# Performance work log

Measured on AMD Instinct MI355X. Metric: run time of the kernel, lower is better.

Reference implementation:

```python
import jax, jax.numpy as jnp
import numpy as np

D_MODEL = 1024
N_HEADS = 16
D_K = D_MODEL // N_HEADS


def setup_inputs() -> dict:
    key = jax.random.key(0)
    ks = jax.random.split(key, 7)
    s = 1.0 / np.sqrt(D_MODEL)
    return {
        "x": jax.random.normal(ks[0], (2, 2048, D_MODEL), dtype=jnp.float32),
        "w_q": jax.random.uniform(ks[1], (D_MODEL, D_MODEL), jnp.float32, -s, s),
        "w_k": jax.random.uniform(ks[2], (D_MODEL, D_MODEL), jnp.float32, -s, s),
        "w_v": jax.random.uniform(ks[3], (D_MODEL, D_MODEL), jnp.float32, -s, s),
        "w_o": jax.random.uniform(ks[4], (D_MODEL, D_MODEL), jnp.float32, -s, s),
        "b_o": jax.random.uniform(ks[5], (D_MODEL,), jnp.float32, -s, s),
        "ln_gamma": jnp.ones((D_MODEL,), jnp.float32),
        "ln_beta": jnp.zeros((D_MODEL,), jnp.float32),
    }


def reference(x, w_q, w_k, w_v, w_o, b_o, ln_gamma, ln_beta):
    # Pre-LN
    mu = jnp.mean(x, axis=-1, keepdims=True)
    var = jnp.mean(jnp.square(x - mu), axis=-1, keepdims=True)
    x_norm = (x - mu) / jnp.sqrt(var + 1e-5) * ln_gamma + ln_beta

    B, S, _ = x.shape
    # torch Linear: y = x @ W.T ; weights stored [out, in]
    def proj(w):
        return (x_norm @ w.T).reshape(B, S, N_HEADS, D_K).transpose(0, 2, 1, 3)

    Q, K, V = proj(w_q), proj(w_k), proj(w_v)  # [B,H,S,Dk]
    scores = jnp.einsum("bhqd,bhkd->bhqk", Q, K) / np.sqrt(D_K)
    attn = jax.nn.softmax(scores, axis=-1)
    attended = jnp.einsum("bhqk,bhkd->bhqd", attn, V)
    attended = attended.transpose(0, 2, 1, 3).reshape(B, S, D_MODEL)
    out = attended @ w_o.T + b_o
    return x + out
```

## Files before the change

### kernel.cpp

```cpp
#include <hip/hip_runtime.h>

typedef _Float16 f16;
typedef _Float16 f16x8 __attribute__((ext_vector_type(8)));
typedef _Float16 f16x4 __attribute__((ext_vector_type(4)));
typedef _Float16 f16x2 __attribute__((ext_vector_type(2)));
typedef __fp16 fp16x2 __attribute__((ext_vector_type(2)));
typedef float f32x4 __attribute__((ext_vector_type(4)));

#define SEQ   2048
#define DM    1024
#define DKH   64
#define MTOT  4096

__device__ __forceinline__ f32x4 mfma16(f16x8 a, f16x8 b, f32x4 c) {
  return __builtin_amdgcn_mfma_f32_16x16x32_f16(a, b, c, 0, 0, 0);
}

__device__ __forceinline__ f16x2 cvt_pk(float a, float b) {
  fp16x2 r = __builtin_amdgcn_cvt_pkrtz(a, b);
  return __builtin_bit_cast(f16x2, r);
}

__device__ __forceinline__ void gload16(const f16* g, f16* l) {
  __builtin_amdgcn_global_load_lds(
      (const __attribute__((address_space(1))) void*)g,
      (__attribute__((address_space(3))) void*)l, 16, 0, 0);
}

__global__ __launch_bounds__(256) void prep_kernel(const float* __restrict__ x,
                                                   const float* __restrict__ w_q,
                                                   const float* __restrict__ w_k,
                                                   const float* __restrict__ w_v,
                                                   const float* __restrict__ w_o,
                                                   const float* __restrict__ gamma,
                                                   const float* __restrict__ beta,
                                                   f16* __restrict__ wout,
                                                   f16* __restrict__ xn) {
  const int t = threadIdx.x;
  if (blockIdx.x < 4096) {
    const int sel = blockIdx.x >> 10;
    const float* src = sel == 0 ? w_q : sel == 1 ? w_k : sel == 2 ? w_v : w_o;
    const int i = ((blockIdx.x & 1023) * 256 + t) * 4;
    float4 v = *reinterpret_cast<const float4*>(src + i);
    f16x4 o;
    o[0] = (f16)v.x; o[1] = (f16)v.y; o[2] = (f16)v.z; o[3] = (f16)v.w;
    *reinterpret_cast<f16x4*>(wout + (size_t)sel * 1048576 + i) = o;
    return;
  }
  const int row = blockIdx.x - 4096;
  const float* xr = x + (size_t)row * DM;
  float v[4], s = 0.f, s2 = 0.f;
#pragma unroll
  for (int i = 0; i < 4; ++i) {
    v[i] = xr[t + i * 256];
    s += v[i];
    s2 += v[i] * v[i];
  }
#pragma unroll
  for (int o = 32; o > 0; o >>= 1) {
    s  += __shfl_down(s, o);
    s2 += __shfl_down(s2, o);
  }
  __shared__ float ps[4], ps2[4], mu_s, rs_s;
  if ((t & 63) == 0) { ps[t >> 6] = s; ps2[t >> 6] = s2; }
  __syncthreads();
  if (t == 0) {
    float a = ps[0] + ps[1] + ps[2] + ps[3];
    float b = ps2[0] + ps2[1] + ps2[2] + ps2[3];
    float mu = a * (1.f / DM);
    float var = b * (1.f / DM) - mu * mu;
    mu_s = mu;
    rs_s = rsqrtf(var + 1e-5f);
  }
  __syncthreads();
  const float mu = mu_s, rs = rs_s;
#pragma unroll
  for (int i = 0; i < 4; ++i) {
    int d = t + i * 256;
    xn[(size_t)row * DM + d] = (f16)(((v[i] - mu) * rs) * gamma[d] + beta[d]);
  }
}

__global__ __launch_bounds__(256) void gemm_qkv(const f16* __restrict__ A,
                                                const f16* __restrict__ Wqkv,
                                                f16* __restrict__ qb,
                                                f16* __restrict__ kb,
                                                f16* __restrict__ vtb) {
  __shared__ f16 sA[128][64];
  __shared__ f16 sB[64][64];
  const int t = threadIdx.x, l = t & 63, w = t >> 6;
  const int wr = w >> 1, wc = w & 1, lg = l >> 4, lm = l & 15;
  const int m0 = blockIdx.y * 128, n0 = blockIdx.x * 64;
  const int crow = l >> 3;
  const int scol = ((l & 7) ^ crow) << 3;
  const int rsw  = (lm & 7) << 3;

  f32x4 acc[4][2] = {};

  for (int k0 = 0; k0 < DM; k0 += 64) {
    __syncthreads();
#pragma unroll
    for (int cc = 0; cc < 4; ++cc) {
      const int c = w + cc * 4;
      gload16(A + (size_t)(m0 + c * 8 + crow) * DM + k0 + scol, &sA[c * 8][0]);
    }
#pragma unroll
    for (int cc = 0; cc < 2; ++cc) {
      const int c = w + cc * 4;
      gload16(Wqkv + (size_t)(n0 + c * 8 + crow) * DM + k0 + scol, &sB[c * 8][0]);
    }
    __syncthreads();
#pragma unroll
    for (int kk = 0; kk < 2; ++kk) {
      f16x8 af[4], bf[2];
#pragma unroll
      for (int i = 0; i < 4; ++i)
        af[i] = *(const f16x8*)&sA[wr * 64 + i * 16 + lm][(kk * 32 + lg * 8) ^ rsw];
#pragma unroll
      for (int i = 0; i < 2; ++i)
        bf[i] = *(const f16x8*)&sB[wc * 32 + i * 16 + lm][(kk * 32 + lg * 8) ^ rsw];
#pragma unroll
      for (int mi = 0; mi < 4; ++mi)
#pragma unroll
        for (int ni = 0; ni < 2; ++ni)
          acc[mi][ni] = mfma16(af[mi], bf[ni], acc[mi][ni]);
    }
  }

  const int sel = blockIdx.x >> 4;
  if (sel < 2) {
    f16* outp = sel == 0 ? qb : kb;
    const int nloc = n0 - sel * 1024;
#pragma unroll
    for (int mi = 0; mi < 4; ++mi) {
      const int rowb = m0 + wr * 64 + mi * 16 + lg * 4;
#pragma unroll
      for (int ni = 0; ni < 2; ++ni) {
        const int col = nloc + wc * 32 + ni * 16 + lm;
#pragma unroll
        for (int r = 0; r < 4; ++r)
          outp[(size_t)(rowb + r) * DM + col] = (f16)acc[mi][ni][r];
      }
    }
  } else {
#pragma unroll
    for (int mi = 0; mi < 4; ++mi) {
      const int rowb = m0 + wr * 64 + mi * 16 + lg * 4;
      const int b = rowb >> 11, s = rowb & 2047;
#pragma unroll
      for (int ni = 0; ni < 2; ++ni) {
        const int col = (n0 - 2048) + wc * 32 + ni * 16 + lm;
        f16x4 o;
        o[0] = (f16)acc[mi][ni][0]; o[1] = (f16)acc[mi][ni][1];
        o[2] = (f16)acc[mi][ni][2]; o[3] = (f16)acc[mi][ni][3];
        *reinterpret_cast<f16x4*>(&vtb[(size_t)(b * 1024 + col) * SEQ + s]) = o;
      }
    }
  }
}

__global__ __launch_bounds__(256) void gemm_out(const f16* __restrict__ A,
                                                const f16* __restrict__ W,
                                                float* __restrict__ out,
                                                const float* __restrict__ bias,
                                                const float* __restrict__ resid) {
  __shared__ f16 sA[64][64];
  __shared__ f16 sB[128][64];
  const int t = threadIdx.x, l = t & 63, w = t >> 6;
  const int wr = w >> 1, wc = w & 1, lg = l >> 4, lm = l & 15;
  const int m0 = blockIdx.y * 64, n0 = blockIdx.x * 128;
  const int crow = l >> 3;
  const int scol = ((l & 7) ^ crow) << 3;
  const int rsw  = (lm & 7) << 3;

  f32x4 acc[2][4] = {};

  for (int k0 = 0; k0 < DM; k0 += 64) {
    __syncthreads();
#pragma unroll
    for (int cc = 0; cc < 2; ++cc) {
      const int c = w + cc * 4;
      gload16(A + (size_t)(m0 + c * 8 + crow) * DM + k0 + scol, &sA[c * 8][0]);
    }
#pragma unroll
    for (int cc = 0; cc < 4; ++cc) {
      const int c = w + cc * 4;
      gload16(W + (size_t)(n0 + c * 8 + crow) * DM + k0 + scol, &sB[c * 8][0]);
    }
    __syncthreads();
#pragma unroll
    for (int kk = 0; kk < 2; ++kk) {
      f16x8 af[2], bf[4];
#pragma unroll
      for (int i = 0; i < 2; ++i)
        af[i] = *(const f16x8*)&sA[wr * 32 + i * 16 + lm][(kk * 32 + lg * 8) ^ rsw];
#pragma unroll
      for (int i = 0; i < 4; ++i)
        bf[i] = *(const f16x8*)&sB[wc * 64 + i * 16 + lm][(kk * 32 + lg * 8) ^ rsw];
#pragma unroll
      for (int mi = 0; mi < 2; ++mi)
#pragma unroll
        for (int ni = 0; ni < 4; ++ni)
          acc[mi][ni] = mfma16(af[mi], bf[ni], acc[mi][ni]);
    }
  }

#pragma unroll
  for (int mi = 0; mi < 2; ++mi) {
    const int rowb = m0 + wr * 32 + mi * 16 + lg * 4;
#pragma unroll
    for (int ni = 0; ni < 4; ++ni) {
      const int col = n0 + wc * 64 + ni * 16 + lm;
#pragma unroll
      for (int r = 0; r < 4; ++r) {
        const size_t idx = (size_t)(rowb + r) * DM + col;
        out[idx] = resid[idx] + bias[col] + acc[mi][ni][r];
      }
    }
  }
}

__global__ __launch_bounds__(256) void attn_kernel(const f16* __restrict__ Qb,
                                                   const f16* __restrict__ Kb,
                                                   const f16* __restrict__ Vt,
                                                   f16* __restrict__ Ob) {
  __shared__ f16 sK[2][128][64];
  __shared__ f16 sV[2][64][128];

  int bx = blockIdx.x;
  bx = (bx & 7) * 64 + (bx >> 3);
  const int qt = bx & 15, bh = bx >> 4;
  const int h = bh & 15, b = bh >> 4;
  const int t = threadIdx.x, l = t & 63, w = t >> 6;
  const int lg = l >> 4, lm = l & 15;
  const float K2 = 0.18033688f;

  f16x8 qf[2][2];
#pragma unroll
  for (int qg = 0; qg < 2; ++qg) {
    const f16* qptr =
        Qb + (size_t)(b * SEQ + qt * 128 + w * 32 + qg * 16 + lm) * DM + h * DKH;
    qf[qg][0] = *(const f16x8*)(qptr + lg * 8);
    qf[qg][1] = *(const f16x8*)(qptr + 32 + lg * 8);
#pragma unroll
    for (int j = 0; j < 8; ++j) {
      qf[qg][0][j] = (f16)((float)qf[qg][0][j] * K2);
      qf[qg][1][j] = (f16)((float)qf[qg][1][j] * K2);
    }
  }

  const f16x8 ones = {(f16)1, (f16)1, (f16)1, (f16)1,
                      (f16)1, (f16)1, (f16)1, (f16)1};

  f32x4 oacc[2][4] = {};
  f32x4 oden[2] = {};

  const int crow = l >> 3;
  const int scol = ((l & 7) ^ crow) << 3;
  const int rsw  = (lm & 7) << 3;

  const f16* kptr[4];
  const f16* vptr[4];
#pragma unroll
  for (int cc = 0; cc < 4; ++cc) {
    const int ck = w + cc * 4;
    const int krow = ck * 8 + crow;
    const int half = krow >> 6, r6 = krow & 63;
    const int nfp = r6 >> 4, lgp = (r6 >> 2) & 3, rp = r6 & 3;
    const int key = half * 64 + (nfp >> 1) * 32 + lgp * 8 + (nfp & 1) * 4 + rp;
    kptr[cc] = Kb + (size_t)(b * SEQ + key) * DM + h * DKH + scol;
    const int drow = ck * 4 + (l >> 4);
    const int vcol = ((l & 15) ^ ((ck & 1) * 4 + (l >> 4))) << 3;
    vptr[cc] = Vt + (size_t)(bh * DKH + drow) * SEQ + vcol;
  }

  auto stage = [&](int buf) {
#pragma unroll
    for (int cc = 0; cc < 4; ++cc) {
      const int ck = w + cc * 4;
      gload16(kptr[cc], &sK[buf][ck * 8][0]);
      gload16(vptr[cc], &sV[buf][ck * 4][0]);
      kptr[cc] += 128 * DM;
      vptr[cc] += 128;
    }
  };

  stage(0);
  __syncthreads();
  int cur = 0;

  for (int kt = 0; kt < SEQ / 128; ++kt) {
    if (kt < SEQ / 128 - 1) stage(cur ^ 1);

#pragma unroll
    for (int half = 0; half < 2; ++half) {
      f32x4 sc[2][4] = {};
      __builtin_amdgcn_s_setprio(1);
#pragma unroll
      for (int kk = 0; kk < 2; ++kk)
#pragma unroll
        for (int nf = 0; nf < 4; ++nf) {
          f16x8 kf = *(const f16x8*)
              &sK[cur][half * 64 + nf * 16 + lm][(kk * 32 + lg * 8) ^ rsw];
          sc[0][nf] = mfma16(kf, qf[0][kk], sc[0][nf]);
          sc[1][nf] = mfma16(kf, qf[1][kk], sc[1][nf]);
        }
      __builtin_amdgcn_s_setprio(0);

      union PU { f16x8 v; f16x2 hh[4]; };
      PU pu[2][2];
#pragma unroll
      for (int qg = 0; qg < 2; ++qg)
#pragma unroll
        for (int nf = 0; nf < 4; ++nf) {
          float e0 = __builtin_amdgcn_exp2f(sc[qg][nf][0]);
          float e1 = __builtin_amdgcn_exp2f(sc[qg][nf][1]);
          float e2 = __builtin_amdgcn_exp2f(sc[qg][nf][2]);
          float e3 = __builtin_amdgcn_exp2f(sc[qg][nf][3]);
          pu[qg][nf >> 1].hh[(nf & 1) * 2 + 0] = cvt_pk(e0, e1);
          pu[qg][nf >> 1].hh[(nf & 1) * 2 + 1] = cvt_pk(e2, e3);
        }

      __builtin_amdgcn_s_setprio(1);
#pragma unroll
      for (int ks = 0; ks < 2; ++ks) {
#pragma unroll
        for (int ni = 0; ni < 4; ++ni) {
          f16x8 vf = *(const f16x8*)
              &sV[cur][ni * 16 + lm][(half * 64 + ks * 32 + lg * 8) ^ rsw];
          oacc[0][ni] = mfma16(pu[0][ks].v, vf, oacc[0][ni]);
          oacc[1][ni] = mfma16(pu[1][ks].v, vf, oacc[1][ni]);
        }
        oden[0] = mfma16(pu[0][ks].v, ones, oden[0]);
        oden[1] = mfma16(pu[1][ks].v, ones, oden[1]);
      }
      __builtin_amdgcn_s_setprio(0);
    }

    __syncthreads();
    cur ^= 1;
  }

#pragma unroll
  for (int qg = 0; qg < 2; ++qg) {
    float rd[4];
#pragma unroll
    for (int r = 0; r < 4; ++r) rd[r] = 1.f / oden[qg][r];
#pragma unroll
    for (int ni = 0; ni < 4; ++ni)
#pragma unroll
      for (int r = 0; r < 4; ++r) {
        const int q = qt * 128 + w * 32 + qg * 16 + lg * 4 + r;
        const int d = ni * 16 + lm;
        Ob[(size_t)(b * SEQ + q) * DM + h * DKH + d] = (f16)(oacc[qg][ni][r] * rd[r]);
      }
  }
}

extern "C" void kernel_launch(void* const* d_in, const int* in_sizes, int n_in,
                              void* d_out, int out_size, void* d_ws, size_t ws_size,
                              hipStream_t stream) {
  const float* x   = (const float*)d_in[0];
  const float* w_q = (const float*)d_in[1];
  const float* w_k = (const float*)d_in[2];
  const float* w_v = (const float*)d_in[3];
  const float* w_o = (const float*)d_in[4];
  const float* b_o = (const float*)d_in[5];
  const float* lng = (const float*)d_in[6];
  const float* lnb = (const float*)d_in[7];
  float* out = (float*)d_out;

  char* ws = (char*)d_ws;
  const size_t MB = 1ull << 20;
  f16* xn   = (f16*)(ws + 0 * MB);
  f16* wqkv = (f16*)(ws + 8 * MB);
  f16* woh  = (f16*)(ws + 14 * MB);
  f16* qb   = (f16*)(ws + 16 * MB);
  f16* kb   = (f16*)(ws + 24 * MB);
  f16* vtb  = (f16*)(ws + 32 * MB);
  f16* att  = (f16*)(ws + 40 * MB);

  prep_kernel<<<8192, 256, 0, stream>>>(x, w_q, w_k, w_v, w_o, lng, lnb, wqkv, xn);
  gemm_qkv<<<dim3(48, 32), 256, 0, stream>>>(xn, wqkv, qb, kb, vtb);
  attn_kernel<<<512, 256, 0, stream>>>(qb, kb, vtb, att);
  gemm_out<<<dim3(8, 64), 256, 0, stream>>>(att, woh, out, b_o, x);
}
```

Baseline: 116.4 us.

## Software-pipeline attention halves, split V tile layout, reshape output GEMM tile

The attention inner loop now preloads the K fragments for both 64-key halves and computes the second half's QK^T MFMAs right after the first half's PV MFMAs. This lets the exp work of one half overlap matrix work of the other. The V shared-memory tile is split into two 64x64 halves with a new swizzled staging pattern. The output GEMM switches from 64x128 to 128x64 block tiles with a matching grid. In exchange, register pressure rises from holding 16 K fragments and a second score accumulator, which may lower occupancy.

```diff
diff --git a/kernel.cpp b/kernel.cpp
--- a/kernel.cpp
+++ b/kernel.cpp
@@ -164,53 +164,53 @@
                                                 float* __restrict__ out,
                                                 const float* __restrict__ bias,
                                                 const float* __restrict__ resid) {
-  __shared__ f16 sA[64][64];
-  __shared__ f16 sB[128][64];
+  __shared__ f16 sA[128][64];
+  __shared__ f16 sB[64][64];
   const int t = threadIdx.x, l = t & 63, w = t >> 6;
   const int wr = w >> 1, wc = w & 1, lg = l >> 4, lm = l & 15;
-  const int m0 = blockIdx.y * 64, n0 = blockIdx.x * 128;
+  const int m0 = blockIdx.y * 128, n0 = blockIdx.x * 64;
   const int crow = l >> 3;
   const int scol = ((l & 7) ^ crow) << 3;
   const int rsw  = (lm & 7) << 3;
 
-  f32x4 acc[2][4] = {};
+  f32x4 acc[4][2] = {};
 
   for (int k0 = 0; k0 < DM; k0 += 64) {
     __syncthreads();
 #pragma unroll
+    for (int cc = 0; cc < 4; ++cc) {
+      const int c = w + cc * 4;
+      gload16(A + (size_t)(m0 + c * 8 + crow) * DM + k0 + scol, &sA[c * 8][0]);
+    }
+#pragma unroll
     for (int cc = 0; cc < 2; ++cc) {
       const int c = w + cc * 4;
-      gload16(A + (size_t)(m0 + c * 8 + crow) * DM + k0 + scol, &sA[c * 8][0]);
-    }
-#pragma unroll
-    for (int cc = 0; cc < 4; ++cc) {
-      const int c = w + cc * 4;
       gload16(W + (size_t)(n0 + c * 8 + crow) * DM + k0 + scol, &sB[c * 8][0]);
     }
     __syncthreads();
 #pragma unroll
     for (int kk = 0; kk < 2; ++kk) {
-      f16x8 af[2], bf[4];
+      f16x8 af[4], bf[2];
+#pragma unroll
+      for (int i = 0; i < 4; ++i)
+        af[i] = *(const f16x8*)&sA[wr * 64 + i * 16 + lm][(kk * 32 + lg * 8) ^ rsw];
 #pragma unroll
       for (int i = 0; i < 2; ++i)
-        af[i] = *(const f16x8*)&sA[wr * 32 + i * 16 + lm][(kk * 32 + lg * 8) ^ rsw];
-#pragma unroll
-      for (int i = 0; i < 4; ++i)
-        bf[i] = *(const f16x8*)&sB[wc * 64 + i * 16 + lm][(kk * 32 + lg * 8) ^ rsw];
-#pragma unroll
-      for (int mi = 0; mi < 2; ++mi)
-#pragma unroll
-        for (int ni = 0; ni < 4; ++ni)
+        bf[i] = *(const f16x8*)&sB[wc * 32 + i * 16 + lm][(kk * 32 + lg * 8) ^ rsw];
+#pragma unroll
+      for (int mi = 0; mi < 4; ++mi)
+#pragma unroll
+        for (int ni = 0; ni < 2; ++ni)
           acc[mi][ni] = mfma16(af[mi], bf[ni], acc[mi][ni]);
     }
   }
 
 #pragma unroll
-  for (int mi = 0; mi < 2; ++mi) {
-    const int rowb = m0 + wr * 32 + mi * 16 + lg * 4;
-#pragma unroll
-    for (int ni = 0; ni < 4; ++ni) {
-      const int col = n0 + wc * 64 + ni * 16 + lm;
+  for (int mi = 0; mi < 4; ++mi) {
+    const int rowb = m0 + wr * 64 + mi * 16 + lg * 4;
+#pragma unroll
+    for (int ni = 0; ni < 2; ++ni) {
+      const int col = n0 + wc * 32 + ni * 16 + lm;
 #pragma unroll
       for (int r = 0; r < 4; ++r) {
         const size_t idx = (size_t)(rowb + r) * DM + col;
@@ -225,7 +225,7 @@
                                                    const f16* __restrict__ Vt,
                                                    f16* __restrict__ Ob) {
   __shared__ f16 sK[2][128][64];
-  __shared__ f16 sV[2][64][128];
+  __shared__ f16 sV[2][2][64][64];
 
   int bx = blockIdx.x;
   bx = (bx & 7) * 64 + (bx >> 3);
@@ -269,9 +269,10 @@
     const int nfp = r6 >> 4, lgp = (r6 >> 2) & 3, rp = r6 & 3;
     const int key = half * 64 + (nfp >> 1) * 32 + lgp * 8 + (nfp & 1) * 4 + rp;
     kptr[cc] = Kb + (size_t)(b * SEQ + key) * DM + h * DKH + scol;
-    const int drow = ck * 4 + (l >> 4);
-    const int vcol = ((l & 15) ^ ((ck & 1) * 4 + (l >> 4))) << 3;
-    vptr[cc] = Vt + (size_t)(bh * DKH + drow) * SEQ + vcol;
+    const int vh = ck & 1, sub = ck >> 1;
+    const int vrow = sub * 8 + (l >> 3);
+    const int vslot = (l & 7) ^ (l >> 3);
+    vptr[cc] = Vt + (size_t)(bh * DKH + vrow) * SEQ + vh * 64 + vslot * 8;
   }
 
   auto stage = [&](int buf) {
@@ -279,7 +280,7 @@
     for (int cc = 0; cc < 4; ++cc) {
       const int ck = w + cc * 4;
       gload16(kptr[cc], &sK[buf][ck * 8][0]);
-      gload16(vptr[cc], &sV[buf][ck * 4][0]);
+      gload16(vptr[cc], &sV[buf][ck & 1][(ck >> 1) * 8][0]);
       kptr[cc] += 128 * DM;
       vptr[cc] += 128;
     }
@@ -289,53 +290,101 @@
   __syncthreads();
   int cur = 0;
 
+  union PU { f16x8 v; f16x2 hh[4]; };
+
   for (int kt = 0; kt < SEQ / 128; ++kt) {
     if (kt < SEQ / 128 - 1) stage(cur ^ 1);
 
-#pragma unroll
-    for (int half = 0; half < 2; ++half) {
-      f32x4 sc[2][4] = {};
-      __builtin_amdgcn_s_setprio(1);
-#pragma unroll
-      for (int kk = 0; kk < 2; ++kk)
-#pragma unroll
-        for (int nf = 0; nf < 4; ++nf) {
-          f16x8 kf = *(const f16x8*)
-              &sK[cur][half * 64 + nf * 16 + lm][(kk * 32 + lg * 8) ^ rsw];
-          sc[0][nf] = mfma16(kf, qf[0][kk], sc[0][nf]);
-          sc[1][nf] = mfma16(kf, qf[1][kk], sc[1][nf]);
-        }
-      __builtin_amdgcn_s_setprio(0);
-
-      union PU { f16x8 v; f16x2 hh[4]; };
-      PU pu[2][2];
-#pragma unroll
-      for (int qg = 0; qg < 2; ++qg)
-#pragma unroll
-        for (int nf = 0; nf < 4; ++nf) {
-          float e0 = __builtin_amdgcn_exp2f(sc[qg][nf][0]);
-          float e1 = __builtin_amdgcn_exp2f(sc[qg][nf][1]);
-          float e2 = __builtin_amdgcn_exp2f(sc[qg][nf][2]);
-          float e3 = __builtin_amdgcn_exp2f(sc[qg][nf][3]);
-          pu[qg][nf >> 1].hh[(nf & 1) * 2 + 0] = cvt_pk(e0, e1);
-          pu[qg][nf >> 1].hh[(nf & 1) * 2 + 1] = cvt_pk(e2, e3);
-        }
-
-      __builtin_amdgcn_s_setprio(1);
-#pragma unroll
-      for (int ks = 0; ks < 2; ++ks) {
-#pragma unroll
-        for (int ni = 0; ni < 4; ++ni) {
-          f16x8 vf = *(const f16x8*)
-              &sV[cur][ni * 16 + lm][(half * 64 + ks * 32 + lg * 8) ^ rsw];
-          oacc[0][ni] = mfma16(pu[0][ks].v, vf, oacc[0][ni]);
-          oacc[1][ni] = mfma16(pu[1][ks].v, vf, oacc[1][ni]);
-        }
-        oden[0] = mfma16(pu[0][ks].v, ones, oden[0]);
-        oden[1] = mfma16(pu[1][ks].v, ones, oden[1]);
-      }
-      __builtin_amdgcn_s_setprio(0);
-    }
+    f16x8 kfa[2][4];
+#pragma unroll
+    for (int kk = 0; kk < 2; ++kk)
+#pragma unroll
+      for (int nf = 0; nf < 4; ++nf)
+        kfa[kk][nf] = *(const f16x8*)
+            &sK[cur][nf * 16 + lm][(kk * 32 + lg * 8) ^ rsw];
+
+    f32x4 sc[2][4] = {};
+    __builtin_amdgcn_s_setprio(1);
+#pragma unroll
+    for (int kk = 0; kk < 2; ++kk)
+#pragma unroll
+      for (int nf = 0; nf < 4; ++nf) {
+        sc[0][nf] = mfma16(kfa[kk][nf], qf[0][kk], sc[0][nf]);
+        sc[1][nf] = mfma16(kfa[kk][nf], qf[1][kk], sc[1][nf]);
+      }
+    __builtin_amdgcn_s_setprio(0);
+
+    f16x8 kfb[2][4];
+#pragma unroll
+    for (int kk = 0; kk < 2; ++kk)
+#pragma unroll
+      for (int nf = 0; nf < 4; ++nf)
+        kfb[kk][nf] = *(const f16x8*)
+            &sK[cur][64 + nf * 16 + lm][(kk * 32 + lg * 8) ^ rsw];
+
+    PU pu[2][2];
+#pragma unroll
+    for (int qg = 0; qg < 2; ++qg)
+#pragma unroll
+      for (int nf = 0; nf < 4; ++nf) {
+        float e0 = __builtin_amdgcn_exp2f(sc[qg][nf][0]);
+        float e1 = __builtin_amdgcn_exp2f(sc[qg][nf][1]);
+        float e2 = __builtin_amdgcn_exp2f(sc[qg][nf][2]);
+        float e3 = __builtin_amdgcn_exp2f(sc[qg][nf][3]);
+        pu[qg][nf >> 1].hh[(nf & 1) * 2 + 0] = cvt_pk(e0, e1);
+        pu[qg][nf >> 1].hh[(nf & 1) * 2 + 1] = cvt_pk(e2, e3);
+      }
+
+    __builtin_amdgcn_s_setprio(1);
+#pragma unroll
+    for (int ks = 0; ks < 2; ++ks) {
+#pragma unroll
+      for (int ni = 0; ni < 4; ++ni) {
+        f16x8 vf = *(const f16x8*)
+            &sV[cur][0][ni * 16 + lm][(ks * 32 + lg * 8) ^ rsw];
+        oacc[0][ni] = mfma16(pu[0][ks].v, vf, oacc[0][ni]);
+        oacc[1][ni] = mfma16(pu[1][ks].v, vf, oacc[1][ni]);
+      }
+      oden[0] = mfma16(pu[0][ks].v, ones, oden[0]);
+      oden[1] = mfma16(pu[1][ks].v, ones, oden[1]);
+    }
+
+    f32x4 sd[2][4] = {};
+#pragma unroll
+    for (int kk = 0; kk < 2; ++kk)
+#pragma unroll
+      for (int nf = 0; nf < 4; ++nf) {
+        sd[0][nf] = mfma16(kfb[kk][nf], qf[0][kk], sd[0][nf]);
+        sd[1][nf] = mfma16(kfb[kk][nf], qf[1][kk], sd[1][nf]);
+      }
+    __builtin_amdgcn_s_setprio(0);
+
+#pragma unroll
+    for (int qg = 0; qg < 2; ++qg)
+#pragma unroll
+      for (int nf = 0; nf < 4; ++nf) {
+        float e0 = __builtin_amdgcn_exp2f(sd[qg][nf][0]);
+        float e1 = __builtin_amdgcn_exp2f(sd[qg][nf][1]);
+        float e2 = __builtin_amdgcn_exp2f(sd[qg][nf][2]);
+        float e3 = __builtin_amdgcn_exp2f(sd[qg][nf][3]);
+        pu[qg][nf >> 1].hh[(nf & 1) * 2 + 0] = cvt_pk(e0, e1);
+        pu[qg][nf >> 1].hh[(nf & 1) * 2 + 1] = cvt_pk(e2, e3);
+      }
+
+    __builtin_amdgcn_s_setprio(1);
+#pragma unroll
+    for (int ks = 0; ks < 2; ++ks) {
+#pragma unroll
+      for (int ni = 0; ni < 4; ++ni) {
+        f16x8 vf = *(const f16x8*)
+            &sV[cur][1][ni * 16 + lm][(ks * 32 + lg * 8) ^ rsw];
+        oacc[0][ni] = mfma16(pu[0][ks].v, vf, oacc[0][ni]);
+        oacc[1][ni] = mfma16(pu[1][ks].v, vf, oacc[1][ni]);
+      }
+      oden[0] = mfma16(pu[0][ks].v, ones, oden[0]);
+      oden[1] = mfma16(pu[1][ks].v, ones, oden[1]);
+    }
+    __builtin_amdgcn_s_setprio(0);
 
     __syncthreads();
     cur ^= 1;
@@ -383,5 +432,5 @@
   prep_kernel<<<8192, 256, 0, stream>>>(x, w_q, w_k, w_v, w_o, lng, lnb, wqkv, xn);
   gemm_qkv<<<dim3(48, 32), 256, 0, stream>>>(xn, wqkv, qb, kb, vtb);
   attn_kernel<<<512, 256, 0, stream>>>(qb, kb, vtb, att);
-  gemm_out<<<dim3(8, 64), 256, 0, stream>>>(att, woh, out, b_o, x);
-}
+  gemm_out<<<dim3(16, 32), 256, 0, stream>>>(att, woh, out, b_o, x);
+}
```

Result: no change. 117.7 us (+1.1%).

## Split attention keys across two wave groups and retile output GEMM

Applied to the files above, without the earlier changes.

The attention kernel now runs 512 threads per block. Two groups of four waves each process half of the key sequence (1024 keys) with 64-key tiles. Their partial numerators and denominators are combined through shared memory at the end, which raises per-block parallelism and shortens each wave's serial loop at the cost of an extra reduction and sync. The output GEMM tile is also changed from 64x128 to 128x64 per block, with the grid adjusted to match.

```diff
diff --git a/kernel.cpp b/kernel.cpp
--- a/kernel.cpp
+++ b/kernel.cpp
@@ -164,53 +164,53 @@
                                                 float* __restrict__ out,
                                                 const float* __restrict__ bias,
                                                 const float* __restrict__ resid) {
-  __shared__ f16 sA[64][64];
-  __shared__ f16 sB[128][64];
+  __shared__ f16 sA[128][64];
+  __shared__ f16 sB[64][64];
   const int t = threadIdx.x, l = t & 63, w = t >> 6;
   const int wr = w >> 1, wc = w & 1, lg = l >> 4, lm = l & 15;
-  const int m0 = blockIdx.y * 64, n0 = blockIdx.x * 128;
+  const int m0 = blockIdx.y * 128, n0 = blockIdx.x * 64;
   const int crow = l >> 3;
   const int scol = ((l & 7) ^ crow) << 3;
   const int rsw  = (lm & 7) << 3;
 
-  f32x4 acc[2][4] = {};
+  f32x4 acc[4][2] = {};
 
   for (int k0 = 0; k0 < DM; k0 += 64) {
     __syncthreads();
 #pragma unroll
+    for (int cc = 0; cc < 4; ++cc) {
+      const int c = w + cc * 4;
+      gload16(A + (size_t)(m0 + c * 8 + crow) * DM + k0 + scol, &sA[c * 8][0]);
+    }
+#pragma unroll
     for (int cc = 0; cc < 2; ++cc) {
       const int c = w + cc * 4;
-      gload16(A + (size_t)(m0 + c * 8 + crow) * DM + k0 + scol, &sA[c * 8][0]);
-    }
-#pragma unroll
-    for (int cc = 0; cc < 4; ++cc) {
-      const int c = w + cc * 4;
       gload16(W + (size_t)(n0 + c * 8 + crow) * DM + k0 + scol, &sB[c * 8][0]);
     }
     __syncthreads();
 #pragma unroll
     for (int kk = 0; kk < 2; ++kk) {
-      f16x8 af[2], bf[4];
+      f16x8 af[4], bf[2];
+#pragma unroll
+      for (int i = 0; i < 4; ++i)
+        af[i] = *(const f16x8*)&sA[wr * 64 + i * 16 + lm][(kk * 32 + lg * 8) ^ rsw];
 #pragma unroll
       for (int i = 0; i < 2; ++i)
-        af[i] = *(const f16x8*)&sA[wr * 32 + i * 16 + lm][(kk * 32 + lg * 8) ^ rsw];
-#pragma unroll
-      for (int i = 0; i < 4; ++i)
-        bf[i] = *(const f16x8*)&sB[wc * 64 + i * 16 + lm][(kk * 32 + lg * 8) ^ rsw];
-#pragma unroll
-      for (int mi = 0; mi < 2; ++mi)
-#pragma unroll
-        for (int ni = 0; ni < 4; ++ni)
+        bf[i] = *(const f16x8*)&sB[wc * 32 + i * 16 + lm][(kk * 32 + lg * 8) ^ rsw];
+#pragma unroll
+      for (int mi = 0; mi < 4; ++mi)
+#pragma unroll
+        for (int ni = 0; ni < 2; ++ni)
           acc[mi][ni] = mfma16(af[mi], bf[ni], acc[mi][ni]);
     }
   }
 
 #pragma unroll
-  for (int mi = 0; mi < 2; ++mi) {
-    const int rowb = m0 + wr * 32 + mi * 16 + lg * 4;
-#pragma unroll
-    for (int ni = 0; ni < 4; ++ni) {
-      const int col = n0 + wc * 64 + ni * 16 + lm;
+  for (int mi = 0; mi < 4; ++mi) {
+    const int rowb = m0 + wr * 64 + mi * 16 + lg * 4;
+#pragma unroll
+    for (int ni = 0; ni < 2; ++ni) {
+      const int col = n0 + wc * 32 + ni * 16 + lm;
 #pragma unroll
       for (int r = 0; r < 4; ++r) {
         const size_t idx = (size_t)(rowb + r) * DM + col;
@@ -220,18 +220,21 @@
   }
 }
 
-__global__ __launch_bounds__(256) void attn_kernel(const f16* __restrict__ Qb,
-                                                   const f16* __restrict__ Kb,
-                                                   const f16* __restrict__ Vt,
-                                                   f16* __restrict__ Ob) {
-  __shared__ f16 sK[2][128][64];
-  __shared__ f16 sV[2][64][128];
+__global__ __launch_bounds__(512, 4) void attn_kernel(const f16* __restrict__ Qb,
+                                                      const f16* __restrict__ Kb,
+                                                      const f16* __restrict__ Vt,
+                                                      f16* __restrict__ Ob) {
+  __shared__ __align__(16) char smem[65536];
+  f16 (*sK)[2][64][64] = (f16(*)[2][64][64])smem;
+  f16 (*sV)[2][64][64] = (f16(*)[2][64][64])(smem + 32768);
+  float* cb = (float*)smem;
 
   int bx = blockIdx.x;
   bx = (bx & 7) * 64 + (bx >> 3);
   const int qt = bx & 15, bh = bx >> 4;
   const int h = bh & 15, b = bh >> 4;
   const int t = threadIdx.x, l = t & 63, w = t >> 6;
+  const int kg = w >> 2, wq = w & 3;
   const int lg = l >> 4, lm = l & 15;
   const float K2 = 0.18033688f;
 
@@ -239,7 +242,7 @@
 #pragma unroll
   for (int qg = 0; qg < 2; ++qg) {
     const f16* qptr =
-        Qb + (size_t)(b * SEQ + qt * 128 + w * 32 + qg * 16 + lm) * DM + h * DKH;
+        Qb + (size_t)(b * SEQ + qt * 128 + wq * 32 + qg * 16 + lm) * DM + h * DKH;
     qf[qg][0] = *(const f16x8*)(qptr + lg * 8);
     qf[qg][1] = *(const f16x8*)(qptr + 32 + lg * 8);
 #pragma unroll
@@ -259,29 +262,26 @@
   const int scol = ((l & 7) ^ crow) << 3;
   const int rsw  = (lm & 7) << 3;
 
-  const f16* kptr[4];
-  const f16* vptr[4];
-#pragma unroll
-  for (int cc = 0; cc < 4; ++cc) {
-    const int ck = w + cc * 4;
-    const int krow = ck * 8 + crow;
-    const int half = krow >> 6, r6 = krow & 63;
-    const int nfp = r6 >> 4, lgp = (r6 >> 2) & 3, rp = r6 & 3;
-    const int key = half * 64 + (nfp >> 1) * 32 + lgp * 8 + (nfp & 1) * 4 + rp;
-    kptr[cc] = Kb + (size_t)(b * SEQ + key) * DM + h * DKH + scol;
-    const int drow = ck * 4 + (l >> 4);
-    const int vcol = ((l & 15) ^ ((ck & 1) * 4 + (l >> 4))) << 3;
-    vptr[cc] = Vt + (size_t)(bh * DKH + drow) * SEQ + vcol;
+  const f16* kptr[2];
+  const f16* vptr[2];
+#pragma unroll
+  for (int cc = 0; cc < 2; ++cc) {
+    const int c = wq + cc * 4;
+    const int krow = c * 8 + crow;
+    const int nfp = krow >> 4, lgp = (krow >> 2) & 3, rp = krow & 3;
+    const int key = (nfp >> 1) * 32 + lgp * 8 + (nfp & 1) * 4 + rp;
+    kptr[cc] = Kb + (size_t)(b * SEQ + kg * 1024 + key) * DM + h * DKH + scol;
+    vptr[cc] = Vt + (size_t)(bh * DKH + c * 8 + crow) * SEQ + kg * 1024 + scol;
   }
 
   auto stage = [&](int buf) {
 #pragma unroll
-    for (int cc = 0; cc < 4; ++cc) {
-      const int ck = w + cc * 4;
-      gload16(kptr[cc], &sK[buf][ck * 8][0]);
-      gload16(vptr[cc], &sV[buf][ck * 4][0]);
-      kptr[cc] += 128 * DM;
-      vptr[cc] += 128;
+    for (int cc = 0; cc < 2; ++cc) {
+      const int c = wq + cc * 4;
+      gload16(kptr[cc], &sK[kg][buf][c * 8][0]);
+      gload16(vptr[cc], &sV[kg][buf][c * 8][0]);
+      kptr[cc] += 64 * DM;
+      vptr[cc] += 64;
     }
   };
 
@@ -289,71 +289,91 @@
   __syncthreads();
   int cur = 0;
 
-  for (int kt = 0; kt < SEQ / 128; ++kt) {
-    if (kt < SEQ / 128 - 1) stage(cur ^ 1);
-
-#pragma unroll
-    for (int half = 0; half < 2; ++half) {
-      f32x4 sc[2][4] = {};
-      __builtin_amdgcn_s_setprio(1);
-#pragma unroll
-      for (int kk = 0; kk < 2; ++kk)
-#pragma unroll
-        for (int nf = 0; nf < 4; ++nf) {
-          f16x8 kf = *(const f16x8*)
-              &sK[cur][half * 64 + nf * 16 + lm][(kk * 32 + lg * 8) ^ rsw];
-          sc[0][nf] = mfma16(kf, qf[0][kk], sc[0][nf]);
-          sc[1][nf] = mfma16(kf, qf[1][kk], sc[1][nf]);
-        }
-      __builtin_amdgcn_s_setprio(0);
-
-      union PU { f16x8 v; f16x2 hh[4]; };
-      PU pu[2][2];
-#pragma unroll
-      for (int qg = 0; qg < 2; ++qg)
-#pragma unroll
-        for (int nf = 0; nf < 4; ++nf) {
-          float e0 = __builtin_amdgcn_exp2f(sc[qg][nf][0]);
-          float e1 = __builtin_amdgcn_exp2f(sc[qg][nf][1]);
-          float e2 = __builtin_amdgcn_exp2f(sc[qg][nf][2]);
-          float e3 = __builtin_amdgcn_exp2f(sc[qg][nf][3]);
-          pu[qg][nf >> 1].hh[(nf & 1) * 2 + 0] = cvt_pk(e0, e1);
-          pu[qg][nf >> 1].hh[(nf & 1) * 2 + 1] = cvt_pk(e2, e3);
-        }
-
-      __builtin_amdgcn_s_setprio(1);
-#pragma unroll
-      for (int ks = 0; ks < 2; ++ks) {
-#pragma unroll
-        for (int ni = 0; ni < 4; ++ni) {
-          f16x8 vf = *(const f16x8*)
-              &sV[cur][ni * 16 + lm][(half * 64 + ks * 32 + lg * 8) ^ rsw];
-          oacc[0][ni] = mfma16(pu[0][ks].v, vf, oacc[0][ni]);
-          oacc[1][ni] = mfma16(pu[1][ks].v, vf, oacc[1][ni]);
-        }
-        oden[0] = mfma16(pu[0][ks].v, ones, oden[0]);
-        oden[1] = mfma16(pu[1][ks].v, ones, oden[1]);
-      }
-      __builtin_amdgcn_s_setprio(0);
-    }
+  union PU { f16x8 v; f16x2 hh[4]; };
+
+  for (int kt = 0; kt < 16; ++kt) {
+    if (kt < 15) stage(cur ^ 1);
+
+    f32x4 sc[2][4] = {};
+    __builtin_amdgcn_s_setprio(1);
+#pragma unroll
+    for (int kk = 0; kk < 2; ++kk)
+#pragma unroll
+      for (int nf = 0; nf < 4; ++nf) {
+        f16x8 kf = *(const f16x8*)
+            &sK[kg][cur][nf * 16 + lm][(kk * 32 + lg * 8) ^ rsw];
+        sc[0][nf] = mfma16(kf, qf[0][kk], sc[0][nf]);
+        sc[1][nf] = mfma16(kf, qf[1][kk], sc[1][nf]);
+      }
+    __builtin_amdgcn_s_setprio(0);
+
+    PU pu[2][2];
+#pragma unroll
+    for (int qg = 0; qg < 2; ++qg)
+#pragma unroll
+      for (int nf = 0; nf < 4; ++nf) {
+        float e0 = __builtin_amdgcn_exp2f(sc[qg][nf][0]);
+        float e1 = __builtin_amdgcn_exp2f(sc[qg][nf][1]);
+        float e2 = __builtin_amdgcn_exp2f(sc[qg][nf][2]);
+        float e3 = __builtin_amdgcn_exp2f(sc[qg][nf][3]);
+        pu[qg][nf >> 1].hh[(nf & 1) * 2 + 0] = cvt_pk(e0, e1);
+        pu[qg][nf >> 1].hh[(nf & 1) * 2 + 1] = cvt_pk(e2, e3);
+      }
+
+    __builtin_amdgcn_s_setprio(1);
+#pragma unroll
+    for (int ks = 0; ks < 2; ++ks) {
+#pragma unroll
+      for (int ni = 0; ni < 4; ++ni) {
+        f16x8 vf = *(const f16x8*)
+            &sV[kg][cur][ni * 16 + lm][(ks * 32 + lg * 8) ^ rsw];
+        oacc[0][ni] = mfma16(pu[0][ks].v, vf, oacc[0][ni]);
+        oacc[1][ni] = mfma16(pu[1][ks].v, vf, oacc[1][ni]);
+      }
+      oden[0] = mfma16(pu[0][ks].v, ones, oden[0]);
+      oden[1] = mfma16(pu[1][ks].v, ones, oden[1]);
+    }
+    __builtin_amdgcn_s_setprio(0);
 
     __syncthreads();
     cur ^= 1;
   }
 
-#pragma unroll
-  for (int qg = 0; qg < 2; ++qg) {
-    float rd[4];
-#pragma unroll
-    for (int r = 0; r < 4; ++r) rd[r] = 1.f / oden[qg][r];
-#pragma unroll
-    for (int ni = 0; ni < 4; ++ni)
-#pragma unroll
-      for (int r = 0; r < 4; ++r) {
-        const int q = qt * 128 + w * 32 + qg * 16 + lg * 4 + r;
-        const int d = ni * 16 + lm;
-        Ob[(size_t)(b * SEQ + q) * DM + h * DKH + d] = (f16)(oacc[qg][ni][r] * rd[r]);
-      }
+  float* myp = cb + (size_t)(wq * 64 + l) * 40;
+  if (kg == 1) {
+#pragma unroll
+    for (int qg = 0; qg < 2; ++qg)
+#pragma unroll
+      for (int ni = 0; ni < 4; ++ni)
+#pragma unroll
+        for (int r = 0; r < 4; ++r) myp[qg * 16 + ni * 4 + r] = oacc[qg][ni][r];
+#pragma unroll
+    for (int qg = 0; qg < 2; ++qg)
+#pragma unroll
+      for (int r = 0; r < 4; ++r) myp[32 + qg * 4 + r] = oden[qg][r];
+  }
+  __syncthreads();
+  if (kg == 0) {
+#pragma unroll
+    for (int qg = 0; qg < 2; ++qg) {
+#pragma unroll
+      for (int ni = 0; ni < 4; ++ni)
+#pragma unroll
+        for (int r = 0; r < 4; ++r) oacc[qg][ni][r] += myp[qg * 16 + ni * 4 + r];
+      float rd[4];
+#pragma unroll
+      for (int r = 0; r < 4; ++r)
+        rd[r] = 1.f / (oden[qg][r] + myp[32 + qg * 4 + r]);
+#pragma unroll
+      for (int ni = 0; ni < 4; ++ni)
+#pragma unroll
+        for (int r = 0; r < 4; ++r) {
+          const int q = qt * 128 + wq * 32 + qg * 16 + lg * 4 + r;
+          const int d = ni * 16 + lm;
+          Ob[(size_t)(b * SEQ + q) * DM + h * DKH + d] =
+              (f16)(oacc[qg][ni][r] * rd[r]);
+        }
+    }
   }
 }
 
@@ -382,6 +402,6 @@
 
   prep_kernel<<<8192, 256, 0, stream>>>(x, w_q, w_k, w_v, w_o, lng, lnb, wqkv, xn);
   gemm_qkv<<<dim3(48, 32), 256, 0, stream>>>(xn, wqkv, qb, kb, vtb);
-  attn_kernel<<<512, 256, 0, stream>>>(qb, kb, vtb, att);
-  gemm_out<<<dim3(8, 64), 256, 0, stream>>>(att, woh, out, b_o, x);
-}
+  attn_kernel<<<512, 512, 0, stream>>>(qb, kb, vtb, att);
+  gemm_out<<<dim3(16, 32), 256, 0, stream>>>(att, woh, out, b_o, x);
+}
```

Measured after the change: 108.5 us. 6.8% less time.
